# Kernel tuning notes

Measured on AMD Instinct MI355X. Metric: run time of the kernel, lower is better.

## Reference

```python
import jax, jax.numpy as jnp
import numpy as np

N_NODES = 50000
N_EDGES = 800000
N_ENTS = 200000
N_RELS = 500
D = 128


def setup_inputs() -> dict:
    key = jax.random.key(0)
    ks = jax.random.split(key, 9)
    return {
        "prev_ent_embs": jax.random.normal(ks[0], (N_ENTS, D), dtype=jnp.float32),
        "rel_embs": jax.random.normal(ks[1], (N_RELS, D), dtype=jnp.float32),
        "loop_weight": jax.random.normal(ks[2], (D, D), dtype=jnp.float32) * 0.1,
        "evolve_loop_weight": jax.random.normal(ks[3], (D, D), dtype=jnp.float32) * 0.1,
        "weight_neighbor": jax.random.normal(ks[4], (D, D), dtype=jnp.float32) * 0.1,
        "node_id": jax.random.randint(ks[5], (N_NODES,), 0, N_ENTS, dtype=jnp.int64) if jax.config.jax_enable_x64 else jax.random.randint(ks[5], (N_NODES,), 0, N_ENTS, dtype=jnp.int32),
        "src": jax.random.randint(ks[6], (N_EDGES,), 0, N_NODES, dtype=jnp.int32),
        "dst": jax.random.randint(ks[7], (N_EDGES,), 0, N_NODES, dtype=jnp.int32),
        "etype": jax.random.randint(ks[8], (N_EDGES,), 0, N_RELS, dtype=jnp.int32),
    }


def reference(prev_ent_embs, rel_embs, loop_weight, evolve_loop_weight,
              weight_neighbor, node_id, src, dst, etype):
    n_nodes = node_id.shape[0]
    # node features gathered from global entity table
    h = prev_ent_embs[node_id]                                    # [N, D]

    # per-edge message: (h[src] + rel[type]) @ W_neighbor
    msg = (h[src] + rel_embs[etype]) @ weight_neighbor            # [E, D]

    # scatter-sum into destination nodes
    agg = jax.ops.segment_sum(msg, dst, num_segments=n_nodes)     # [N, D]

    # in-degree and norm (apply_func: h * in_norm, standard 1/in_degree)
    deg = jax.ops.segment_sum(jnp.ones_like(dst, dtype=h.dtype), dst,
                              num_segments=n_nodes)               # [N]
    has_in = deg > 0
    in_norm = jnp.where(has_in, 1.0 / jnp.maximum(deg, 1.0), 0.0)[:, None]
    agg = agg * in_norm

    # self-loop: loop_weight where in_degree>0, evolve_loop_weight otherwise
    loop_msg = jnp.where(has_in[:, None], h @ loop_weight, h @ evolve_loop_weight)

    # activation (dropout=0 -> identity in eval)
    return jax.nn.relu(agg + loop_msg)
```

## Files before the change

kernel.cpp:

```cpp
#include <hip/hip_runtime.h>
#include <hip/hip_bf16.h>
#include <stdint.h>

#define N_NODES 50000
#define N_EDGES 800000
#define N_ENTS  200000
#define N_RELS  500
#define DIM     128

#define DEGS 32
#define CAP  64

#define ZERO_REC ((int)(50000u | (500u << 16)))

using f32x4  = __attribute__((ext_vector_type(4))) float;
using bf16x8 = __attribute__((ext_vector_type(8))) short;

static __device__ __forceinline__ ushort f_to_bf16(float f) {
    __hip_bfloat16 h = __float2bfloat16(f);
    return *reinterpret_cast<ushort*>(&h);
}
static __device__ __forceinline__ uint pack2(float a, float b) {
    return (uint)f_to_bf16(a) | ((uint)f_to_bf16(b) << 16);
}
static __device__ __forceinline__ float blo(uint u) { return __uint_as_float(u << 16); }
static __device__ __forceinline__ float bhi(uint u) { return __uint_as_float(u & 0xffff0000u); }

__global__ __launch_bounds__(256) void k_front(
        const float* __restrict__ prev, const int* __restrict__ node_id,
        ushort* __restrict__ afull,
        const int* __restrict__ dst, const int* __restrict__ src,
        const int* __restrict__ etype,
        int* __restrict__ deg, uint* __restrict__ srcpk,
        const float* __restrict__ rel, ushort* __restrict__ rel_bf,
        const float* __restrict__ Wn, const float* __restrict__ Wl,
        ushort* __restrict__ WfT) {
    int blk = blockIdx.x;
    if (blk < 3125) {
        int e = blk * 256 + threadIdx.x;
        if (e < N_EDGES) {
            int dn = dst[e];
            uint rec = (uint)src[e] | ((uint)etype[e] << 16);
            int r = atomicAdd(&deg[dn * DEGS], 1);
            if (r < CAP) srcpk[dn * CAP + r] = rec;
        }
    } else if (blk < 6250) {
        int i = (blk - 3125) * 256 + threadIdx.x;
        int row = i >> 4, c = (i & 15) * 8;
        int nid = node_id[row];
        const float* p = prev + (size_t)nid * DIM + c;
        float4 v0 = *(const float4*)p;
        float4 v1 = *(const float4*)(p + 4);
        uint4 w;
        w.x = pack2(v0.x, v0.y);
        w.y = pack2(v0.z, v0.w);
        w.z = pack2(v1.x, v1.y);
        w.w = pack2(v1.z, v1.w);
        *(uint4*)(afull + (size_t)row * 256 + 128 + c) = w;
    } else if (blk < 6504) {
        int i = (blk - 6250) * 256 + threadIdx.x;
        if (i < 128 * 256) {
            int n = i >> 8, k = i & 255;
            float v = (k < 128) ? Wn[k * 128 + n] : Wl[(k - 128) * 128 + n];
            WfT[i] = f_to_bf16(v);
        } else {
            int j = i - 128 * 256;
            if (j < N_RELS * 64) {
                float2 v = *(const float2*)(rel + j * 2);
                *(uint*)(rel_bf + j * 2) = pack2(v.x, v.y);
            }
        }
    } else {
        int t = threadIdx.x;
        if (t < 128)       ((uint*)(afull + (size_t)50000 * 256))[t] = 0u;
        else if (t < 192)  ((uint*)(rel_bf + 500 * 128))[t - 128]    = 0u;
    }
}

__global__ __launch_bounds__(256) void k_agg(ushort* __restrict__ afull,
                                             const ushort* __restrict__ rel_bf,
                                             const uint* __restrict__ srcpk,
                                             const int* __restrict__ deg) {
    int wave = threadIdx.x >> 6, lane = threadIdx.x & 63;
    int n = blockIdx.x * 4 + wave;
    if (n >= N_NODES) return;
    int d = deg[n * DEGS];
    int cnt = min(d, CAP);
    int g = lane >> 4, q = lane & 15;
    const ushort* hb = afull + 128 + q * 8;
    const ushort* rb = rel_bf + q * 8;
    float acc[8] = {0.f, 0.f, 0.f, 0.f, 0.f, 0.f, 0.f, 0.f};

#define ACC4(hv, rv)                                              \
    acc[0] += blo(hv.x) + blo(rv.x); acc[1] += bhi(hv.x) + bhi(rv.x); \
    acc[2] += blo(hv.y) + blo(rv.y); acc[3] += bhi(hv.y) + bhi(rv.y); \
    acc[4] += blo(hv.z) + blo(rv.z); acc[5] += bhi(hv.z) + bhi(rv.z); \
    acc[6] += blo(hv.w) + blo(rv.w); acc[7] += bhi(hv.w) + bhi(rv.w);

    int rec = (lane < cnt) ? (int)srcpk[n * CAP + lane] : ZERO_REC;
    for (int j = 0; j < cnt; j += 16) {
        uint e0 = (uint)__shfl(rec, j + g);
        uint e1 = (uint)__shfl(rec, j + 4 + g);
        uint e2 = (uint)__shfl(rec, j + 8 + g);
        uint e3 = (uint)__shfl(rec, j + 12 + g);
        uint4 h0 = *(const uint4*)(hb + (size_t)(e0 & 0xffffu) * 256);
        uint4 r0 = *(const uint4*)(rb + (e0 >> 16) * 128);
        uint4 h1 = *(const uint4*)(hb + (size_t)(e1 & 0xffffu) * 256);
        uint4 r1 = *(const uint4*)(rb + (e1 >> 16) * 128);
        uint4 h2 = *(const uint4*)(hb + (size_t)(e2 & 0xffffu) * 256);
        uint4 r2 = *(const uint4*)(rb + (e2 >> 16) * 128);
        uint4 h3 = *(const uint4*)(hb + (size_t)(e3 & 0xffffu) * 256);
        uint4 r3 = *(const uint4*)(rb + (e3 >> 16) * 128);
        ACC4(h0, r0);
        ACC4(h1, r1);
        ACC4(h2, r2);
        ACC4(h3, r3);
    }
#undef ACC4

#pragma unroll
    for (int i = 0; i < 8; i++) {
        acc[i] += __shfl_xor(acc[i], 16);
        acc[i] += __shfl_xor(acc[i], 32);
    }
    float norm = (d > 0) ? 1.0f / (float)d : 0.0f;
    if (g == 0) {
        uint4 w;
        w.x = pack2(acc[0] * norm, acc[1] * norm);
        w.y = pack2(acc[2] * norm, acc[3] * norm);
        w.z = pack2(acc[4] * norm, acc[5] * norm);
        w.w = pack2(acc[6] * norm, acc[7] * norm);
        *(uint4*)(afull + (size_t)n * 256 + q * 8) = w;
    }
}

#define LDSK 264
__global__ __launch_bounds__(256) void k_mm(const ushort* __restrict__ afull,
                                            const ushort* __restrict__ WfT,
                                            const int* __restrict__ deg,
                                            const float* __restrict__ We,
                                            float* __restrict__ out) {
    __shared__ ushort wl[128 * LDSK];
    for (int idx = threadIdx.x; idx < 128 * 32; idx += 256) {
        int n = idx >> 5, p = idx & 31;
        uint4 v = *(const uint4*)(WfT + n * 256 + p * 8);
        *(uint4*)(&wl[n * LDSK + p * 8]) = v;
    }
    __syncthreads();

    int wave = threadIdx.x >> 6, lane = threadIdx.x & 63;
    int m = lane & 15, quad = lane >> 4;
    int rowBase = blockIdx.x * 128 + wave * 32;

    f32x4 acc[2][8];
#pragma unroll
    for (int rt = 0; rt < 2; rt++)
#pragma unroll
        for (int ct = 0; ct < 8; ct++) acc[rt][ct] = f32x4{0.f, 0.f, 0.f, 0.f};

    int r0 = rowBase + m;      if (r0 > N_NODES - 1) r0 = N_NODES - 1;
    int r1 = rowBase + 16 + m; if (r1 > N_NODES - 1) r1 = N_NODES - 1;
    const ushort* pa0 = afull + (size_t)r0 * 256 + quad * 8;
    const ushort* pa1 = afull + (size_t)r1 * 256 + quad * 8;

#pragma unroll
    for (int ks = 0; ks < 8; ks++) {
        bf16x8 a0 = *(const bf16x8*)(pa0 + ks * 32);
        bf16x8 a1 = *(const bf16x8*)(pa1 + ks * 32);
#pragma unroll
        for (int ct = 0; ct < 8; ct++) {
            bf16x8 b = *(const bf16x8*)(&wl[(ct * 16 + m) * LDSK + ks * 32 + quad * 8]);
            acc[0][ct] = __builtin_amdgcn_mfma_f32_16x16x32_bf16(a0, b, acc[0][ct], 0, 0, 0);
            acc[1][ct] = __builtin_amdgcn_mfma_f32_16x16x32_bf16(a1, b, acc[1][ct], 0, 0, 0);
        }
    }

#pragma unroll
    for (int rt = 0; rt < 2; rt++) {
        int rbase = rowBase + rt * 16 + quad * 4;
#pragma unroll
        for (int reg = 0; reg < 4; reg++) {
            int grow = rbase + reg;
            if (grow < N_NODES) {
                if (__builtin_expect(deg[grow * DEGS] == 0, 0)) {
#pragma unroll 1
                    for (int ct = 0; ct < 8; ct++) {
                        int col = ct * 16 + m;
                        float a = 0.f;
#pragma unroll 1
                        for (int k = 0; k < 128; k++) {
                            float hv = blo((uint)afull[(size_t)grow * 256 + 128 + k]);
                            a += hv * We[k * 128 + col];
                        }
                        out[(size_t)grow * 128 + col] = a > 0.f ? a : 0.f;
                    }
                } else {
#pragma unroll
                    for (int ct = 0; ct < 8; ct++) {
                        float v = acc[rt][ct][reg];
                        out[(size_t)grow * 128 + ct * 16 + m] = v > 0.f ? v : 0.f;
                    }
                }
            }
        }
    }
}

extern "C" void kernel_launch(void* const* d_in, const int* in_sizes, int n_in,
                              void* d_out, int out_size, void* d_ws, size_t ws_size,
                              hipStream_t stream) {
    const float* prev  = (const float*)d_in[0];
    const float* rel   = (const float*)d_in[1];
    const float* Wl    = (const float*)d_in[2];
    const float* We    = (const float*)d_in[3];
    const float* Wn    = (const float*)d_in[4];
    const int* node_id = (const int*)d_in[5];
    const int* src     = (const int*)d_in[6];
    const int* dst     = (const int*)d_in[7];
    const int* etype   = (const int*)d_in[8];
    float* out = (float*)d_out;

    char* ws = (char*)d_ws;
    ushort* afull  = (ushort*)(ws);
    ushort* WfT    = (ushort*)(ws + 25600512);
    ushort* rel_bf = (ushort*)(ws + 25666048);
    int* deg       = (int*)(ws + 25794304);
    uint* srcpk    = (uint*)(ws + 32194304);

    hipMemsetAsync(deg, 0, 6400000, stream);
    k_front <<<6505,  256, 0, stream>>>(prev, node_id, afull, dst, src, etype,
                                        deg, srcpk, rel, rel_bf, Wn, Wl, WfT);
    k_agg   <<<12500, 256, 0, stream>>>(afull, rel_bf, srcpk, deg);
    k_mm    <<<391,   256, 0, stream>>>(afull, WfT, deg, We, out);
}
```

Before: 241.8 us.

## Split front kernel, use packed float2 accumulation and 4-edge tail loop in aggregation

Splits the combined front kernel into a separate edge-bucketing kernel and a gather/convert kernel, adding one launch on the same stream. The aggregation kernel now accumulates in two-wide float vectors, which may let the compiler use packed FP32 adds. Its main loop handles only full 16-edge groups, and a remainder loop steps by 4 edges so padded dummy records are loaded less often. The extra launch adds overhead and takes away the overlap of the atomic edge work with the gather work inside one grid.

```diff
diff --git a/kernel.cpp b/kernel.cpp
--- a/kernel.cpp
+++ b/kernel.cpp
@@ -14,6 +14,7 @@
 #define ZERO_REC ((int)(50000u | (500u << 16)))
 
 using f32x4  = __attribute__((ext_vector_type(4))) float;
+using f32x2  = __attribute__((ext_vector_type(2))) float;
 using bf16x8 = __attribute__((ext_vector_type(8))) short;
 
 static __device__ __forceinline__ ushort f_to_bf16(float f) {
@@ -24,28 +25,32 @@
     return (uint)f_to_bf16(a) | ((uint)f_to_bf16(b) << 16);
 }
 static __device__ __forceinline__ float blo(uint u) { return __uint_as_float(u << 16); }
-static __device__ __forceinline__ float bhi(uint u) { return __uint_as_float(u & 0xffff0000u); }
-
-__global__ __launch_bounds__(256) void k_front(
+static __device__ __forceinline__ f32x2 up2(uint u) {
+    return f32x2{__uint_as_float(u << 16), __uint_as_float(u & 0xffff0000u)};
+}
+
+__global__ __launch_bounds__(256) void k_edge(
+        const int* __restrict__ dst, const int* __restrict__ src,
+        const int* __restrict__ etype,
+        int* __restrict__ deg, uint* __restrict__ srcpk) {
+    int e = blockIdx.x * 256 + threadIdx.x;
+    if (e < N_EDGES) {
+        int dn = dst[e];
+        uint rec = (uint)src[e] | ((uint)etype[e] << 16);
+        int r = atomicAdd(&deg[dn * DEGS], 1);
+        if (r < CAP) srcpk[dn * CAP + r] = rec;
+    }
+}
+
+__global__ __launch_bounds__(256) void k_rest(
         const float* __restrict__ prev, const int* __restrict__ node_id,
         ushort* __restrict__ afull,
-        const int* __restrict__ dst, const int* __restrict__ src,
-        const int* __restrict__ etype,
-        int* __restrict__ deg, uint* __restrict__ srcpk,
         const float* __restrict__ rel, ushort* __restrict__ rel_bf,
         const float* __restrict__ Wn, const float* __restrict__ Wl,
         ushort* __restrict__ WfT) {
     int blk = blockIdx.x;
     if (blk < 3125) {
-        int e = blk * 256 + threadIdx.x;
-        if (e < N_EDGES) {
-            int dn = dst[e];
-            uint rec = (uint)src[e] | ((uint)etype[e] << 16);
-            int r = atomicAdd(&deg[dn * DEGS], 1);
-            if (r < CAP) srcpk[dn * CAP + r] = rec;
-        }
-    } else if (blk < 6250) {
-        int i = (blk - 3125) * 256 + threadIdx.x;
+        int i = blk * 256 + threadIdx.x;
         int row = i >> 4, c = (i & 15) * 8;
         int nid = node_id[row];
         const float* p = prev + (size_t)nid * DIM + c;
@@ -57,8 +62,8 @@
         w.z = pack2(v1.x, v1.y);
         w.w = pack2(v1.z, v1.w);
         *(uint4*)(afull + (size_t)row * 256 + 128 + c) = w;
-    } else if (blk < 6504) {
-        int i = (blk - 6250) * 256 + threadIdx.x;
+    } else if (blk < 3379) {
+        int i = (blk - 3125) * 256 + threadIdx.x;
         if (i < 128 * 256) {
             int n = i >> 8, k = i & 255;
             float v = (k < 128) ? Wn[k * 128 + n] : Wl[(k - 128) * 128 + n];
@@ -89,16 +94,17 @@
     int g = lane >> 4, q = lane & 15;
     const ushort* hb = afull + 128 + q * 8;
     const ushort* rb = rel_bf + q * 8;
-    float acc[8] = {0.f, 0.f, 0.f, 0.f, 0.f, 0.f, 0.f, 0.f};
-
-#define ACC4(hv, rv)                                              \
-    acc[0] += blo(hv.x) + blo(rv.x); acc[1] += bhi(hv.x) + bhi(rv.x); \
-    acc[2] += blo(hv.y) + blo(rv.y); acc[3] += bhi(hv.y) + bhi(rv.y); \
-    acc[4] += blo(hv.z) + blo(rv.z); acc[5] += bhi(hv.z) + bhi(rv.z); \
-    acc[6] += blo(hv.w) + blo(rv.w); acc[7] += bhi(hv.w) + bhi(rv.w);
+    f32x2 ac0 = {0.f, 0.f}, ac1 = {0.f, 0.f}, ac2 = {0.f, 0.f}, ac3 = {0.f, 0.f};
+
+#define ACCP(hv, rv)                        \
+    ac0 += up2(hv.x) + up2(rv.x);           \
+    ac1 += up2(hv.y) + up2(rv.y);           \
+    ac2 += up2(hv.z) + up2(rv.z);           \
+    ac3 += up2(hv.w) + up2(rv.w);
 
     int rec = (lane < cnt) ? (int)srcpk[n * CAP + lane] : ZERO_REC;
-    for (int j = 0; j < cnt; j += 16) {
+    int j = 0;
+    for (; j + 16 <= cnt; j += 16) {
         uint e0 = (uint)__shfl(rec, j + g);
         uint e1 = (uint)__shfl(rec, j + 4 + g);
         uint e2 = (uint)__shfl(rec, j + 8 + g);
@@ -111,13 +117,20 @@
         uint4 r2 = *(const uint4*)(rb + (e2 >> 16) * 128);
         uint4 h3 = *(const uint4*)(hb + (size_t)(e3 & 0xffffu) * 256);
         uint4 r3 = *(const uint4*)(rb + (e3 >> 16) * 128);
-        ACC4(h0, r0);
-        ACC4(h1, r1);
-        ACC4(h2, r2);
-        ACC4(h3, r3);
-    }
-#undef ACC4
-
+        ACCP(h0, r0);
+        ACCP(h1, r1);
+        ACCP(h2, r2);
+        ACCP(h3, r3);
+    }
+    for (int s = j; s < cnt; s += 4) {
+        uint e = (uint)__shfl(rec, s + g);
+        uint4 h = *(const uint4*)(hb + (size_t)(e & 0xffffu) * 256);
+        uint4 r = *(const uint4*)(rb + (e >> 16) * 128);
+        ACCP(h, r);
+    }
+#undef ACCP
+
+    float acc[8] = {ac0.x, ac0.y, ac1.x, ac1.y, ac2.x, ac2.y, ac3.x, ac3.y};
 #pragma unroll
     for (int i = 0; i < 8; i++) {
         acc[i] += __shfl_xor(acc[i], 16);
@@ -228,8 +241,8 @@
     uint* srcpk    = (uint*)(ws + 32194304);
 
     hipMemsetAsync(deg, 0, 6400000, stream);
-    k_front <<<6505,  256, 0, stream>>>(prev, node_id, afull, dst, src, etype,
-                                        deg, srcpk, rel, rel_bf, Wn, Wl, WfT);
-    k_agg   <<<12500, 256, 0, stream>>>(afull, rel_bf, srcpk, deg);
-    k_mm    <<<391,   256, 0, stream>>>(afull, WfT, deg, We, out);
-}
+    k_edge <<<3125,  256, 0, stream>>>(dst, src, etype, deg, srcpk);
+    k_rest <<<3380,  256, 0, stream>>>(prev, node_id, afull, rel, rel_bf, Wn, Wl, WfT);
+    k_agg  <<<12500, 256, 0, stream>>>(afull, rel_bf, srcpk, deg);
+    k_mm   <<<391,   256, 0, stream>>>(afull, WfT, deg, We, out);
+}
```

Result: slower. 252.7 us (+4.5%).
